# Performance work log

Hardware: AMD Instinct MI355X
Metric: run time of the kernel (lower is better)

The kernel has to match this reference:

```python
import jax, jax.numpy as jnp
import numpy as np

NUM_EMBEDDINGS = 1024
EMBEDDING_DIM = 64


def setup_inputs() -> dict:
    key = jax.random.key(0)
    k1, k2 = jax.random.split(key)
    z = jax.random.normal(k1, (64, 32, 32, EMBEDDING_DIM), dtype=jnp.float32)
    # torch init: uniform_(-1/num_embeddings, 1/num_embeddings)
    lim = 1.0 / NUM_EMBEDDINGS
    codebook = jax.random.uniform(
        k2, (NUM_EMBEDDINGS, EMBEDDING_DIM), dtype=jnp.float32,
        minval=-lim, maxval=lim)
    return {"z": z, "codebook": codebook}


def reference(z, codebook):
    # z: [..., D]; codebook: [K, D]
    z_flat = z.reshape(-1, z.shape[-1])                      # [N, D]
    # ||z||^2 - 2 z.e + ||e||^2  -> [N, K]
    distances = (
        jnp.sum(z_flat ** 2, axis=1, keepdims=True)
        - 2.0 * jnp.einsum("nd,kd->nk", z_flat, codebook)
        + jnp.sum(codebook ** 2, axis=1)
    )
    min_indices = jnp.argmin(distances, axis=1)              # [N]
    z_q = jnp.take(codebook, min_indices, axis=0).reshape(z.shape)
    return z_q, min_indices
```

## Files before the change

kernel.cpp:

```cpp
#include <hip/hip_runtime.h>
#include <hip/hip_bf16.h>
#include <math.h>


#define D      64
#define K      1024
#define BR     64
#define BLOCK  64

typedef _Float16 half8_t __attribute__((ext_vector_type(8)));
typedef float    floatx4 __attribute__((ext_vector_type(4)));
typedef unsigned long long u64;

#define WS_KEYS_OFF  0
#define WS_CN_OFF    524288
#define WS_EF_OFF    528384

__device__ __forceinline__ float np_sumsq64_p(const float* __restrict__ x) {
    float r[8];
    {
        float4 v0 = *(const float4*)(x);
        float4 v1 = *(const float4*)(x + 4);
        r[0] = __fmul_rn(v0.x, v0.x); r[1] = __fmul_rn(v0.y, v0.y);
        r[2] = __fmul_rn(v0.z, v0.z); r[3] = __fmul_rn(v0.w, v0.w);
        r[4] = __fmul_rn(v1.x, v1.x); r[5] = __fmul_rn(v1.y, v1.y);
        r[6] = __fmul_rn(v1.z, v1.z); r[7] = __fmul_rn(v1.w, v1.w);
    }
#pragma unroll
    for (int i = 8; i < 64; i += 8) {
        float4 v0 = *(const float4*)(x + i);
        float4 v1 = *(const float4*)(x + i + 4);
        r[0] = __fadd_rn(r[0], __fmul_rn(v0.x, v0.x));
        r[1] = __fadd_rn(r[1], __fmul_rn(v0.y, v0.y));
        r[2] = __fadd_rn(r[2], __fmul_rn(v0.z, v0.z));
        r[3] = __fadd_rn(r[3], __fmul_rn(v0.w, v0.w));
        r[4] = __fadd_rn(r[4], __fmul_rn(v1.x, v1.x));
        r[5] = __fadd_rn(r[5], __fmul_rn(v1.y, v1.y));
        r[6] = __fadd_rn(r[6], __fmul_rn(v1.z, v1.z));
        r[7] = __fadd_rn(r[7], __fmul_rn(v1.w, v1.w));
    }
    return __fadd_rn(__fadd_rn(__fadd_rn(r[0], r[1]), __fadd_rn(r[2], r[3])),
                     __fadd_rn(__fadd_rn(r[4], r[5]), __fadd_rn(r[6], r[7])));
}

__global__ void vq_pre(const float* __restrict__ cb, float* __restrict__ cn,
                       _Float16* __restrict__ ef) {
    const int k = blockIdx.x * 64 + threadIdx.x;
    if (k >= K) return;
    cn[k] = np_sumsq64_p(cb + (long)k * D);
    const int t = k >> 6, ct = (k >> 4) & 3, l16 = k & 15;
#pragma unroll
    for (int ch = 0; ch < 2; ++ch)
#pragma unroll
        for (int quad = 0; quad < 4; ++quad) {
            const float* p = cb + (long)k * D + ch * 32 + quad * 8;
            half8_t h1, h2;
#pragma unroll
            for (int j = 0; j < 8; ++j) {
                float x10 = __fmul_rn(p[j], 1024.0f);
                _Float16 g1 = (_Float16)x10;
                h1[j] = g1;
                h2[j] = (_Float16)(__fmul_rn(__fsub_rn(x10, (float)g1), 2048.0f));
            }
            const int base = t * 8192 + 128 * quad + 8 * l16;
            *(half8_t*)(ef + base + 512 * (ch * 4 + ct))       = h1;
            *(half8_t*)(ef + base + 512 * ((2 + ch) * 4 + ct)) = h2;
        }
}

__global__ __launch_bounds__(BLOCK, 2) void vq_main(
    const float* __restrict__ z, const _Float16* __restrict__ ef,
    const float* __restrict__ cn, u64* __restrict__ keys) {
    __shared__ __align__(16) float zf[BR * 68];
    __shared__ float sS[BR];
    __shared__ float sCn[512];

    const int lane = threadIdx.x;
    const int quad = lane >> 4;
    const int l16  = lane & 15;
    const int rb = blockIdx.x >> 1, ks = blockIdx.x & 1;
    const long rowbase = (long)rb * BR;
    const int kb0 = ks * 512;

    const float4* gz = (const float4*)(z + rowbase * D);
#pragma unroll
    for (int i = 0; i < 16; ++i) {
        int idx4 = i * BLOCK + lane;
        int r = idx4 >> 4, j = idx4 & 15;
        *(float4*)(zf + r * 68 + j * 4) = gz[idx4];
    }
#pragma unroll
    for (int i = 0; i < 8; ++i) sCn[i * 64 + lane] = cn[kb0 + i * 64 + lane];
    __syncthreads();

    sS[lane] = np_sumsq64_p(zf + lane * 68);

    half8_t a1[4][2], a2[4][2];
#pragma unroll
    for (int rt = 0; rt < 4; ++rt) {
        const int row = rt * 16 + l16;
#pragma unroll
        for (int ch = 0; ch < 2; ++ch) {
            const float* p = zf + row * 68 + ch * 32 + quad * 8;
            float4 f0 = *(const float4*)(p);
            float4 f1 = *(const float4*)(p + 4);
            float xs[8] = {f0.x, f0.y, f0.z, f0.w, f1.x, f1.y, f1.z, f1.w};
#pragma unroll
            for (int j = 0; j < 8; ++j) {
                _Float16 h1 = (_Float16)xs[j];
                a1[rt][ch][j] = h1;
                a2[rt][ch][j] =
                    (_Float16)(__fmul_rn(__fsub_rn(xs[j], (float)h1), 2048.0f));
            }
        }
    }
    __syncthreads();

    float myS[4][4];
#pragma unroll
    for (int rt = 0; rt < 4; ++rt)
#pragma unroll
        for (int r = 0; r < 4; ++r)
            myS[rt][r] = sS[rt * 16 + quad * 4 + r];

    float bv[4][4];
    int   bi[4][4];
#pragma unroll
    for (int rt = 0; rt < 4; ++rt)
#pragma unroll
        for (int r = 0; r < 4; ++r) { bv[rt][r] = INFINITY; bi[rt][r] = 0; }

    const _Float16* eb = ef + (long)ks * 8 * 8192;

    for (int t = 0; t < 8; ++t) {
        const _Float16* tb = eb + t * 8192 + 8 * lane;
        const int kbase = kb0 + t * 64;
#pragma unroll
        for (int ct = 0; ct < 4; ++ct) {
            half8_t b1[2], b2[2];
#pragma unroll
            for (int ch = 0; ch < 2; ++ch) {
                b1[ch] = *(const half8_t*)(tb + 512 * (ch * 4 + ct));
                b2[ch] = *(const half8_t*)(tb + 512 * ((2 + ch) * 4 + ct));
            }
            const float cnv = sCn[t * 64 + ct * 16 + l16];
            const int kg = kbase + ct * 16 + l16;
#pragma unroll
            for (int rt = 0; rt < 4; ++rt) {
                floatx4 aM = (floatx4){0.f, 0.f, 0.f, 0.f};
                floatx4 aC = (floatx4){0.f, 0.f, 0.f, 0.f};
                aM = __builtin_amdgcn_mfma_f32_16x16x32_f16(a1[rt][0], b1[0], aM, 0, 0, 0);
                aM = __builtin_amdgcn_mfma_f32_16x16x32_f16(a1[rt][1], b1[1], aM, 0, 0, 0);
                aC = __builtin_amdgcn_mfma_f32_16x16x32_f16(a1[rt][0], b2[0], aC, 0, 0, 0);
                aC = __builtin_amdgcn_mfma_f32_16x16x32_f16(a1[rt][1], b2[1], aC, 0, 0, 0);
                aC = __builtin_amdgcn_mfma_f32_16x16x32_f16(a2[rt][0], b1[0], aC, 0, 0, 0);
                aC = __builtin_amdgcn_mfma_f32_16x16x32_f16(a2[rt][1], b1[1], aC, 0, 0, 0);
#pragma unroll
                for (int r = 0; r < 4; ++r) {
                    float ds = fmaf(aC[r], 0x1p-11f, aM[r]);
                    float t2 = __fmul_rn(ds, 0x1p-9f);
                    float dist = __fadd_rn(__fsub_rn(myS[rt][r], t2), cnv);
                    if (dist < bv[rt][r]) { bv[rt][r] = dist; bi[rt][r] = kg; }
                }
            }
        }
    }

#pragma unroll
    for (int rt = 0; rt < 4; ++rt)
#pragma unroll
        for (int r = 0; r < 4; ++r) {
            float v = bv[rt][r];
            int   x = bi[rt][r];
#pragma unroll
            for (int off = 1; off <= 8; off <<= 1) {
                float ov = __shfl_xor(v, off);
                int   ox = __shfl_xor(x, off);
                if (ov < v || (ov == v && ox < x)) { v = ov; x = ox; }
            }
            if (l16 == 0) {
                const long row = rowbase + rt * 16 + quad * 4 + r;
                u64 key = ((u64)__float_as_uint(v) << 32) | (unsigned)x;
                atomicMin(&keys[row], key);
            }
        }
}

__global__ void vq_resolve(const float* __restrict__ cb,
                           const u64* __restrict__ keys,
                           float* __restrict__ zq, float* __restrict__ idx_out) {
    const int gid = blockIdx.x * 256 + threadIdx.x;
    const int row = gid >> 4, j = gid & 15;
    const unsigned k = (unsigned)(keys[row] & 0xFFFFFFFFu);
    ((float4*)zq)[gid] = ((const float4*)cb)[(long)k * 16 + j];
    if (j == 0) idx_out[row] = (float)k;
}

extern "C" void kernel_launch(void* const* d_in, const int* in_sizes, int n_in,
                              void* d_out, int out_size, void* d_ws, size_t ws_size,
                              hipStream_t stream) {
    const float* z  = (const float*)d_in[0];
    const float* cb = (const float*)d_in[1];

    const int n_rows = in_sizes[0] / D;
    float* zq      = (float*)d_out;
    float* idx_out = zq + (long)n_rows * D;

    u64*      ws_keys = (u64*)((char*)d_ws + WS_KEYS_OFF);
    float*    ws_cn   = (float*)((char*)d_ws + WS_CN_OFF);
    _Float16* ws_ef   = (_Float16*)((char*)d_ws + WS_EF_OFF);

    hipMemsetAsync(ws_keys, 0xFF, (size_t)n_rows * sizeof(u64), stream);
    vq_pre<<<K / 64, 64, 0, stream>>>(cb, ws_cn, ws_ef);
    vq_main<<<(n_rows / BR) * 2, BLOCK, 0, stream>>>(z, ws_ef, ws_cn, ws_keys);
    vq_resolve<<<(n_rows * 16) / 256, 256, 0, stream>>>(cb, ws_keys, zq, idx_out);
}
```

Measured before the change: 111.5 us.

## Share codebook tiles across four waves via double-buffered async LDS loads

Blocks grow from one wave to four, each covering 128 rows instead of 64, so every block loads each codebook tile once and the waves share it instead of each wave reading the fp16 split codebook from global memory. Tiles are streamed into LDS with global_load_lds and double-buffered so the next tile is fetched while the current one feeds the MFMAs. The shared memory that held z during setup is reused for the tile buffers. The cost is a block-wide barrier every tile iteration and fewer row tiles per wave.

```diff
diff --git a/kernel.cpp b/kernel.cpp
--- a/kernel.cpp
+++ b/kernel.cpp
@@ -5,8 +5,7 @@
 
 #define D      64
 #define K      1024
-#define BR     64
-#define BLOCK  64
+#define BLOCK  256
 
 typedef _Float16 half8_t __attribute__((ext_vector_type(8)));
 typedef float    floatx4 __attribute__((ext_vector_type(4)));
@@ -15,6 +14,12 @@
 #define WS_KEYS_OFF  0
 #define WS_CN_OFF    524288
 #define WS_EF_OFF    528384
+
+__device__ __forceinline__ void gld_lds16(const void* g, void* l) {
+    __builtin_amdgcn_global_load_lds(
+        (const __attribute__((address_space(1))) void*)g,
+        (__attribute__((address_space(3))) void*)l, 16, 0, 0);
+}
 
 __device__ __forceinline__ float np_sumsq64_p(const float* __restrict__ x) {
     float r[8];
@@ -68,37 +73,41 @@
         }
 }
 
-__global__ __launch_bounds__(BLOCK, 2) void vq_main(
+__global__ __launch_bounds__(BLOCK, 4) void vq_main(
     const float* __restrict__ z, const _Float16* __restrict__ ef,
     const float* __restrict__ cn, u64* __restrict__ keys) {
-    __shared__ __align__(16) float zf[BR * 68];
-    __shared__ float sS[BR];
+    __shared__ __align__(16) char smem[34816];
+    __shared__ float sS[128];
     __shared__ float sCn[512];
-
-    const int lane = threadIdx.x;
+    float*    zf   = (float*)smem;
+    _Float16* bufs = (_Float16*)smem;
+
+    const int tid  = threadIdx.x;
+    const int lane = tid & 63;
+    const int wv   = tid >> 6;
     const int quad = lane >> 4;
     const int l16  = lane & 15;
     const int rb = blockIdx.x >> 1, ks = blockIdx.x & 1;
-    const long rowbase = (long)rb * BR;
+    const long rowbase = (long)rb * 128;
     const int kb0 = ks * 512;
 
     const float4* gz = (const float4*)(z + rowbase * D);
 #pragma unroll
-    for (int i = 0; i < 16; ++i) {
-        int idx4 = i * BLOCK + lane;
+    for (int i = 0; i < 8; ++i) {
+        int idx4 = i * BLOCK + tid;
         int r = idx4 >> 4, j = idx4 & 15;
         *(float4*)(zf + r * 68 + j * 4) = gz[idx4];
     }
-#pragma unroll
-    for (int i = 0; i < 8; ++i) sCn[i * 64 + lane] = cn[kb0 + i * 64 + lane];
+    sCn[tid]       = cn[kb0 + tid];
+    sCn[tid + 256] = cn[kb0 + tid + 256];
     __syncthreads();
 
-    sS[lane] = np_sumsq64_p(zf + lane * 68);
-
-    half8_t a1[4][2], a2[4][2];
-#pragma unroll
-    for (int rt = 0; rt < 4; ++rt) {
-        const int row = rt * 16 + l16;
+    if (tid < 128) sS[tid] = np_sumsq64_p(zf + tid * 68);
+
+    half8_t a1[2][2], a2[2][2];
+#pragma unroll
+    for (int rt = 0; rt < 2; ++rt) {
+        const int row = wv * 32 + rt * 16 + l16;
 #pragma unroll
         for (int ch = 0; ch < 2; ++ch) {
             const float* p = zf + row * 68 + ch * 32 + quad * 8;
@@ -116,24 +125,40 @@
     }
     __syncthreads();
 
-    float myS[4][4];
-#pragma unroll
-    for (int rt = 0; rt < 4; ++rt)
+    float myS[2][4];
+#pragma unroll
+    for (int rt = 0; rt < 2; ++rt)
 #pragma unroll
         for (int r = 0; r < 4; ++r)
-            myS[rt][r] = sS[rt * 16 + quad * 4 + r];
-
-    float bv[4][4];
-    int   bi[4][4];
-#pragma unroll
-    for (int rt = 0; rt < 4; ++rt)
+            myS[rt][r] = sS[wv * 32 + rt * 16 + quad * 4 + r];
+
+    float bv[2][4];
+    int   bi[2][4];
+#pragma unroll
+    for (int rt = 0; rt < 2; ++rt)
 #pragma unroll
         for (int r = 0; r < 4; ++r) { bv[rt][r] = INFINITY; bi[rt][r] = 0; }
 
-    const _Float16* eb = ef + (long)ks * 8 * 8192;
+    const char* eb = (const char*)(ef + (long)ks * 8 * 8192);
+
+    {
+        const char* g = eb + wv * 4096 + lane * 16;
+        char* l = (char*)bufs + wv * 4096;
+#pragma unroll
+        for (int i = 0; i < 4; ++i) gld_lds16(g + i * 1024, l + i * 1024);
+    }
+    __syncthreads();
 
     for (int t = 0; t < 8; ++t) {
-        const _Float16* tb = eb + t * 8192 + 8 * lane;
+        const _Float16* cur = bufs + (t & 1) * 8192;
+        if (t < 7) {
+            const char* g = eb + (t + 1) * 16384 + wv * 4096 + lane * 16;
+            char* l = (char*)bufs + ((t + 1) & 1) * 8192 * 2 + wv * 4096;
+#pragma unroll
+            for (int i = 0; i < 4; ++i) gld_lds16(g + i * 1024, l + i * 1024);
+        }
+
+        const _Float16* tb = cur + 8 * lane;
         const int kbase = kb0 + t * 64;
 #pragma unroll
         for (int ct = 0; ct < 4; ++ct) {
@@ -146,7 +171,7 @@
             const float cnv = sCn[t * 64 + ct * 16 + l16];
             const int kg = kbase + ct * 16 + l16;
 #pragma unroll
-            for (int rt = 0; rt < 4; ++rt) {
+            for (int rt = 0; rt < 2; ++rt) {
                 floatx4 aM = (floatx4){0.f, 0.f, 0.f, 0.f};
                 floatx4 aC = (floatx4){0.f, 0.f, 0.f, 0.f};
                 aM = __builtin_amdgcn_mfma_f32_16x16x32_f16(a1[rt][0], b1[0], aM, 0, 0, 0);
@@ -164,10 +189,11 @@
                 }
             }
         }
-    }
-
-#pragma unroll
-    for (int rt = 0; rt < 4; ++rt)
+        __syncthreads();
+    }
+
+#pragma unroll
+    for (int rt = 0; rt < 2; ++rt)
 #pragma unroll
         for (int r = 0; r < 4; ++r) {
             float v = bv[rt][r];
@@ -179,7 +205,7 @@
                 if (ov < v || (ov == v && ox < x)) { v = ov; x = ox; }
             }
             if (l16 == 0) {
-                const long row = rowbase + rt * 16 + quad * 4 + r;
+                const long row = rowbase + wv * 32 + rt * 16 + quad * 4 + r;
                 u64 key = ((u64)__float_as_uint(v) << 32) | (unsigned)x;
                 atomicMin(&keys[row], key);
             }
@@ -212,6 +238,6 @@
 
     hipMemsetAsync(ws_keys, 0xFF, (size_t)n_rows * sizeof(u64), stream);
     vq_pre<<<K / 64, 64, 0, stream>>>(cb, ws_cn, ws_ef);
-    vq_main<<<(n_rows / BR) * 2, BLOCK, 0, stream>>>(z, ws_ef, ws_cn, ws_keys);
+    vq_main<<<(n_rows / 128) * 2, BLOCK, 0, stream>>>(z, ws_ef, ws_cn, ws_keys);
     vq_resolve<<<(n_rows * 16) / 256, 256, 0, stream>>>(cb, ws_keys, zq, idx_out);
 }
```

Result: slower. 127.8 us (+14.6%).
